# Performance work log

Hardware: AMD Instinct MI355X
Metric: run time of the kernel (lower is better)

## Reference

```python
import jax, jax.numpy as jnp
import numpy as np

B, L, J, CL, CJ, DM, NH, NB, OBS = 8192, 32, 31, 4, 8, 64, 4, 3, 128
TOK = CL * 16  # 64, flattened per-link token size
HD = DM // NH


def _ln(x, g, b):
    m = x.mean(-1, keepdims=True)
    v = ((x - m) ** 2).mean(-1, keepdims=True)
    return (x - m) / jnp.sqrt(v + 1e-5) * g + b


def setup_inputs() -> dict:
    key = jax.random.key(0)
    ks = list(jax.random.split(key, 30))
    rn = lambda k, s, sc=0.05: jax.random.normal(k, s, dtype=jnp.float32) * sc
    inp = {
        'obs': jax.random.normal(ks[0], (B, OBS), dtype=jnp.float32),
        # per-link MLP encoders (obs->64->TOK), stacked over links
        'link_enc_w1': rn(ks[1], (L, 64, OBS)),
        'link_enc_b1': jnp.zeros((L, 64), jnp.float32),
        'link_enc_w2': rn(ks[2], (L, TOK, 64)),
        'link_enc_b2': jnp.zeros((L, TOK), jnp.float32),
        # per-joint encoders (obs->CJ)
        'joint_enc_w': rn(ks[3], (J, CJ, OBS)),
        'joint_enc_b': jnp.zeros((J, CJ), jnp.float32),
        # Rodrigues kernels per block per joint
        'rod_mix': rn(ks[4], (NB, J, CL, CL), 0.2),
        'rod_theta_w': rn(ks[5], (NB, J, CL, CJ), 0.2),
        'rod_theta_b': jnp.zeros((NB, J, CL), jnp.float32),
        'rod_gen': rn(ks[6], (NB, J, 4, 4), 0.2),
        'rod_ln_g': jnp.ones((NB, L, TOK), jnp.float32),
        'rod_ln_b': jnp.zeros((NB, L, TOK), jnp.float32),
        # JointLayer linears per block per joint (TOK->CJ)
        'jl_w': rn(ks[7], (NB, J, CJ, TOK)),
        'jl_b': jnp.zeros((NB, J, CJ), jnp.float32),
        # attention per block
        'proj_in_w': rn(ks[8], (NB, DM, TOK)),
        'proj_in_b': jnp.zeros((NB, DM), jnp.float32),
        'qkv_w': rn(ks[9], (NB, 3 * DM, DM)),
        'qkv_b': jnp.zeros((NB, 3 * DM), jnp.float32),
        'attn_out_w': rn(ks[10], (NB, DM, DM)),
        'attn_out_b': jnp.zeros((NB, DM), jnp.float32),
        'proj_out_w': rn(ks[11], (NB, TOK, DM)),
        'proj_out_b': jnp.zeros((NB, TOK), jnp.float32),
        'attn_ln_g': jnp.ones((NB, TOK), jnp.float32),
        'attn_ln_b': jnp.zeros((NB, TOK), jnp.float32),
        # kinematic chain edges: parent j -> child j+1
        'p_idx': jnp.arange(J, dtype=jnp.int32),
        'c_idx': jnp.arange(1, J + 1, dtype=jnp.int32),
    }
    return inp


def _forward(obs, link_enc_w1, link_enc_b1, link_enc_w2, link_enc_b2,
             joint_enc_w, joint_enc_b, rod_mix, rod_theta_w, rod_theta_b,
             rod_gen, rod_ln_g, rod_ln_b, jl_w, jl_b, proj_in_w, proj_in_b,
             qkv_w, qkv_b, attn_out_w, attn_out_b, proj_out_w, proj_out_b,
             attn_ln_g, attn_ln_b, p_idx, c_idx):
    b = obs.shape[0]
    # ---- encode ----
    h = jax.nn.elu(jnp.einsum('bo,lho->blh', obs, link_enc_w1) + link_enc_b1)
    link = jnp.einsum('blh,lgh->blg', h, link_enc_w2) + link_enc_b2  # (B,L,TOK)
    link = link.reshape(b, L, CL, 4, 4)
    joint = jnp.einsum('bo,jco->bjc', obs, joint_enc_w) + joint_enc_b  # (B,J,CJ)
    for t in range(NB):
        # ---- RodriguesLayer (reads input link feats; unique children -> parallel) ----
        Fp = link[:, p_idx]  # (B,J,CL,4,4)
        Fc = link[:, c_idx]
        Fm = jnp.einsum('joc,bjcxy->bjoxy', rod_mix[t], Fp)
        a = jnp.einsum('bjc,joc->bjo', joint, rod_theta_w[t]) + rod_theta_b[t]  # (B,J,CL)
        G = rod_gen[t]
        GF = jnp.einsum('jxy,bjoyz->bjoxz', G, Fm)
        GGF = jnp.einsum('jxy,bjoyz->bjoxz', G, GF)
        s = jnp.sin(a)[..., None, None]
        c1 = (1.0 - jnp.cos(a))[..., None, None]
        Ft = Fm + s * GF + c1 * GGF  # Rodrigues: F + sin(a) G F + (1-cos(a)) G^2 F
        comb = _ln((Fc + Ft).reshape(b, J, TOK), rod_ln_g[t][c_idx], rod_ln_b[t][c_idx])
        root = _ln(link[:, 0].reshape(b, TOK), rod_ln_g[t][0], rod_ln_b[t][0])
        link = link.at[:, 0].set(root.reshape(b, CL, 4, 4))
        link = link.at[:, c_idx].set(comb.reshape(b, J, CL, 4, 4))
        # ---- JointLayer ----
        child_flat = link[:, c_idx].reshape(b, J, TOK)
        joint = jnp.einsum('bjh,jch->bjc', child_flat, jl_w[t]) + jl_b[t] + joint
        # ---- SelfAttentionLayer ----
        tok = link.reshape(b, L, TOK)
        x = jnp.einsum('blh,dh->bld', tok, proj_in_w[t]) + proj_in_b[t]
        qkv = jnp.einsum('bld,ed->ble', x, qkv_w[t]) + qkv_b[t]
        q, k, v = jnp.split(qkv, 3, axis=-1)
        hsplit = lambda z: z.reshape(b, L, NH, HD).transpose(0, 2, 1, 3)
        q, k, v = hsplit(q), hsplit(k), hsplit(v)
        attn = jax.nn.softmax(jnp.einsum('bhqd,bhkd->bhqk', q, k) / jnp.sqrt(jnp.float32(HD)), axis=-1)
        o = jnp.einsum('bhqk,bhkd->bhqd', attn, v).transpose(0, 2, 1, 3).reshape(b, L, DM)
        o = jnp.einsum('bld,ed->ble', o, attn_out_w[t]) + attn_out_b[t]
        o = jnp.einsum('bld,hd->blh', o, proj_out_w[t]) + proj_out_b[t]
        tok = _ln(tok + o, attn_ln_g[t], attn_ln_b[t])
        link = tok.reshape(b, L, CL, 4, 4)
    return jnp.concatenate([link.reshape(b, -1), joint.reshape(b, -1)], axis=-1)


def reference(obs, link_enc_w1, link_enc_b1, link_enc_w2, link_enc_b2,
              joint_enc_w, joint_enc_b, rod_mix, rod_theta_w, rod_theta_b,
              rod_gen, rod_ln_g, rod_ln_b, jl_w, jl_b, proj_in_w, proj_in_b,
              qkv_w, qkv_b, attn_out_w, attn_out_b, proj_out_w, proj_out_b,
              attn_ln_g, attn_ln_b, p_idx, c_idx):
    return _forward(obs, link_enc_w1, link_enc_b1, link_enc_w2, link_enc_b2,
                    joint_enc_w, joint_enc_b, rod_mix, rod_theta_w, rod_theta_b,
                    rod_gen, rod_ln_g, rod_ln_b, jl_w, jl_b, proj_in_w, proj_in_b,
                    qkv_w, qkv_b, attn_out_w, attn_out_b, proj_out_w, proj_out_b,
                    attn_ln_g, attn_ln_b, p_idx, c_idx)
```

## Files before the change

kernel.cpp:

```cpp
#include <hip/hip_runtime.h>

typedef unsigned short u16;
typedef __attribute__((ext_vector_type(8))) short bh8;
typedef __attribute__((ext_vector_type(4))) float fx4;

__device__ __forceinline__ u16 f2b(float f){
  unsigned int u = __float_as_uint(f);
  u += 0x7fffu + ((u>>16)&1u);
  return (u16)(u>>16);
}
__device__ __forceinline__ float b2f(u16 h){
  return __uint_as_float(((unsigned int)h)<<16);
}
__device__ __forceinline__ bh8 ldf(const u16* p){
  return *(const bh8*)p;
}
#define MFMA(a,b,c) __builtin_amdgcn_mfma_f32_16x16x32_bf16((a),(b),(c),0,0,0)

static const long OFF_W1 = 0;
static const long OFF_W2 = 278528;
static const long OFF_WJ = 425984;
static const long OFF_PI = 460800;
static const long OFF_QK = 474624;
static const long OFF_AO = 516096;
static const long OFF_PO = 529920;
static const long WS_U16 = 543744;

__global__ __launch_bounds__(256) void conv_kernel(
  const float* __restrict__ w1, const float* __restrict__ w2,
  const float* __restrict__ wj, const float* __restrict__ pi,
  const float* __restrict__ qk, const float* __restrict__ ao,
  const float* __restrict__ po, u16* __restrict__ ws)
{
  const int stride = gridDim.x*blockDim.x;
  const int g0 = blockIdx.x*blockDim.x + threadIdx.x;
  for (int i=g0;i<2048*136;i+=stride){ int r=i/136,c=i-r*136; ws[OFF_W1+i]= (c<128)? f2b(w1[(long)r*128+c]) : (u16)0; }
  for (int i=g0;i<2048*72;i+=stride){ int r=i/72,c=i-r*72; ws[OFF_W2+i]= (c<64)? f2b(w2[(long)(r<<6)+c]) : (u16)0; }
  for (int i=g0;i<256*136;i+=stride){ int r=i/136,c=i-r*136; ws[OFF_WJ+i]= (c<128&&r<248)? f2b(wj[(long)(r<<7)+c]) : (u16)0; }
  for (int i=g0;i<192*72;i+=stride){ int r=i/72,c=i-r*72; ws[OFF_PI+i]= (c<64)? f2b(pi[(r<<6)+c]) : (u16)0; }
  for (int i=g0;i<576*72;i+=stride){ int r=i/72,c=i-r*72; ws[OFF_QK+i]= (c<64)? f2b(qk[(r<<6)+c]) : (u16)0; }
  for (int i=g0;i<192*72;i+=stride){ int r=i/72,c=i-r*72; ws[OFF_AO+i]= (c<64)? f2b(ao[(r<<6)+c]) : (u16)0; }
  for (int i=g0;i<192*72;i+=stride){ int r=i/72,c=i-r*72; ws[OFF_PO+i]= (c<64)? f2b(po[(r<<6)+c]) : (u16)0; }
}

struct __align__(16) SMem1 {
  u16 obs_l[16][136];
  u16 wa[64][136];
  u16 wb[64][72];
  u16 hb[16][72];
};

template<bool PRE>
__global__ __launch_bounds__(256) void enc_kernel(
  const float* __restrict__ obs, const float* __restrict__ w1,
  const float* __restrict__ b1, const float* __restrict__ w2,
  const float* __restrict__ b2, const float* __restrict__ wj,
  const float* __restrict__ bj, const u16* __restrict__ wsw,
  float* __restrict__ dout)
{
  __shared__ SMem1 s;
  const int tid = threadIdx.x;
  const int wave = tid>>6, lane = tid&63;
  const int g = lane>>4, cc = lane&15;
  const long bb = (long)blockIdx.x*16;

  for (int i=tid;i<16*128;i+=256){ int r=i>>7,c=i&127; s.obs_l[r][c]=f2b(obs[(bb+r)*128+c]); }

  for (int l=0;l<32;l++){
    if (PRE){
      const u16* s1 = wsw + OFF_W1 + (long)l*8704;
      for (int i=tid*8;i<8704;i+=2048) *(bh8*)(&s.wa[0][0]+i) = *(const bh8*)(s1+i);
      const u16* s2 = wsw + OFF_W2 + (long)l*4608;
      for (int i=tid*8;i<4608;i+=2048) *(bh8*)(&s.wb[0][0]+i) = *(const bh8*)(s2+i);
    } else {
      for (int i=tid;i<64*128;i+=256){ s.wa[i>>7][i&127]=f2b(w1[(long)l*8192+i]); }
      for (int i=tid;i<64*64;i+=256){ s.wb[i>>6][i&63]=f2b(w2[(long)l*4096+i]); }
    }
    __syncthreads();
    {
      fx4 acc = {0.f,0.f,0.f,0.f};
      #pragma unroll
      for (int ks=0;ks<4;ks++)
        acc = MFMA(ldf(&s.obs_l[cc][ks*32+g*8]), ldf(&s.wa[wave*16+cc][ks*32+g*8]), acc);
      int col = wave*16+cc;
      float bias = b1[l*64+col];
      #pragma unroll
      for (int r=0;r<4;r++){
        float v = acc[r]+bias;
        v = v>0.f ? v : expm1f(v);
        s.hb[g*4+r][col] = f2b(v);
      }
    }
    __syncthreads();
    {
      fx4 acc = {0.f,0.f,0.f,0.f};
      #pragma unroll
      for (int ks=0;ks<2;ks++)
        acc = MFMA(ldf(&s.hb[cc][ks*32+g*8]), ldf(&s.wb[wave*16+cc][ks*32+g*8]), acc);
      int col = wave*16+cc;
      float bias = b2[l*64+col];
      #pragma unroll
      for (int r=0;r<4;r++)
        dout[(bb+g*4+r)*2296 + l*64 + col] = acc[r]+bias;
    }
    __syncthreads();
  }
  for (int ci=0;ci<4;ci++){
    if (PRE){
      const u16* sj = wsw + OFF_WJ + (long)ci*8704;
      for (int i=tid*8;i<8704;i+=2048) *(bh8*)(&s.wa[0][0]+i) = *(const bh8*)(sj+i);
    } else {
      for (int i=tid;i<64*128;i+=256){
        int r=i>>7,c=i&127; int grow=ci*64+r;
        s.wa[r][c] = (grow<248)? f2b(wj[(long)grow*128+c]) : (u16)0;
      }
    }
    __syncthreads();
    fx4 acc={0.f,0.f,0.f,0.f};
    #pragma unroll
    for (int ks=0;ks<4;ks++)
      acc = MFMA(ldf(&s.obs_l[cc][ks*32+g*8]), ldf(&s.wa[wave*16+cc][ks*32+g*8]), acc);
    int ncol = ci*64 + wave*16 + cc;
    if (ncol<248){
      float bias = bj[ncol];
      #pragma unroll
      for (int r=0;r<4;r++)
        dout[(bb+g*4+r)*2296 + 2048 + ncol] = acc[r]+bias;
    }
    __syncthreads();
  }
}

struct __align__(16) SMem2 {
  float tokf[4][32][68];
  u16   tokb[4][32][72];
  u16   xs[4*32*72];
  u16   qs[4*32*72];
  u16   kk[4*32*72];
  u16   vT[4][64][40];
  float joint[4][31][8];
  union {
    u16 w[192*72];
    u16 p[8][32][40];
  } u;
};
static_assert(sizeof(SMem2) <= 163840, "LDS overflow");

template<int NT, class EPI>
__device__ __forceinline__ void gemm8(const u16* A, const u16* W,
                                      int wave, int lane, EPI epi){
  const int g = lane>>4, cc = lane&15;
  const int row = wave*16 + cc;
  bh8 a0 = ldf(&A[row*72 + g*8]);
  bh8 a1 = ldf(&A[row*72 + 32 + g*8]);
  #pragma unroll
  for (int nt=0;nt<NT;nt++){
    bh8 b0 = ldf(&W[(nt*16+cc)*72 + g*8]);
    bh8 b1 = ldf(&W[(nt*16+cc)*72 + 32 + g*8]);
    fx4 acc = {0.f,0.f,0.f,0.f};
    acc = MFMA(a0,b0,acc);
    acc = MFMA(a1,b1,acc);
    epi(nt, wave, acc);
  }
}

template<bool PRE>
__device__ __forceinline__ void stageW(u16* dst, const u16* wsrc, const float* fsrc, int rows){
  if (PRE){
    const int n = rows*72;
    for (int i=threadIdx.x*8; i<n; i+=4096)
      *(bh8*)(dst+i) = *(const bh8*)(wsrc+i);
  } else {
    const int n = rows*64;
    for (int i=threadIdx.x; i<n; i+=512)
      dst[(i>>6)*72 + (i&63)] = f2b(fsrc[i]);
  }
}

template<bool PRE>
__global__ __launch_bounds__(512,1) void rodri_main(
  const float* __restrict__ rod_mix, const float* __restrict__ rod_theta_w,
  const float* __restrict__ rod_theta_b, const float* __restrict__ rod_gen,
  const float* __restrict__ rod_ln_g, const float* __restrict__ rod_ln_b,
  const float* __restrict__ jl_w, const float* __restrict__ jl_b,
  const float* __restrict__ proj_in_w, const float* __restrict__ proj_in_b,
  const float* __restrict__ qkv_w, const float* __restrict__ qkv_b,
  const float* __restrict__ attn_out_w, const float* __restrict__ attn_out_b,
  const float* __restrict__ proj_out_w, const float* __restrict__ proj_out_b,
  const float* __restrict__ attn_ln_g, const float* __restrict__ attn_ln_b,
  const u16* __restrict__ wsw, float* __restrict__ dout)
{
  __shared__ SMem2 s;
  const int tid = threadIdx.x;
  const int wave = tid>>6, lane = tid&63;
  const int g = lane>>4, cc = lane&15;
  const long bb = (long)blockIdx.x*4;

  for (int i=tid;i<4*2048;i+=512){
    int b=i>>11, r=i&2047;
    float v = dout[(bb+b)*2296 + r];
    s.tokf[b][r>>6][r&63] = v;
    s.tokb[b][r>>6][r&63] = f2b(v);
  }
  for (int i=tid;i<4*248;i+=512){
    int b=i/248, r=i-b*248;
    s.joint[b][r>>3][r&7] = dout[(bb+b)*2296 + 2048 + r];
  }
  __syncthreads();

  for (int t=0;t<3;t++){
    {
      const int unit = tid>>2, o = tid&3;
      const int b = unit>>5, row = unit&31;
      float nv[16];
      if (row == 0){
        #pragma unroll
        for (int i=0;i<16;i++) nv[i] = s.tokf[b][0][o*16+i];
      } else {
        const int j = row-1;
        const long wj = (long)t*31 + j;
        const float* mixp = rod_mix + wj*16 + o*4;
        const float* thwp = rod_theta_w + wj*32 + o*8;
        const float* genp = rod_gen + wj*16;
        float a = rod_theta_b[wj*4+o];
        #pragma unroll
        for (int c8=0;c8<8;c8++) a += s.joint[b][j][c8]*thwp[c8];
        float sn = sinf(a), c1 = 1.f - cosf(a);
        const float m0 = mixp[0], m1 = mixp[1], m2 = mixp[2], m3 = mixp[3];
        float G[16];
        #pragma unroll
        for (int e=0;e<16;e++) G[e] = genp[e];
        #pragma unroll
        for (int z=0;z<4;z++){
          float fm[4], gf[4], gg[4];
          #pragma unroll
          for (int x=0;x<4;x++)
            fm[x] = m0*s.tokf[b][j][     x*4+z] + m1*s.tokf[b][j][16 + x*4+z]
                  + m2*s.tokf[b][j][32 + x*4+z] + m3*s.tokf[b][j][48 + x*4+z];
          #pragma unroll
          for (int x=0;x<4;x++)
            gf[x] = G[x*4+0]*fm[0] + G[x*4+1]*fm[1] + G[x*4+2]*fm[2] + G[x*4+3]*fm[3];
          #pragma unroll
          for (int x=0;x<4;x++)
            gg[x] = G[x*4+0]*gf[0] + G[x*4+1]*gf[1] + G[x*4+2]*gf[2] + G[x*4+3]*gf[3];
          #pragma unroll
          for (int x=0;x<4;x++)
            nv[x*4+z] = fm[x] + sn*gf[x] + c1*gg[x] + s.tokf[b][row][o*16+x*4+z];
        }
      }
      float sum=0.f, ssq=0.f;
      #pragma unroll
      for (int i=0;i<16;i++){ sum+=nv[i]; ssq+=nv[i]*nv[i]; }
      sum += __shfl_xor(sum,1); ssq += __shfl_xor(ssq,1);
      sum += __shfl_xor(sum,2); ssq += __shfl_xor(ssq,2);
      float mean = sum*(1.f/64.f);
      float var  = ssq*(1.f/64.f) - mean*mean;
      float rstd = rsqrtf(var + 1e-5f);
      const float* lng = rod_ln_g + ((long)t*32+row)*64 + o*16;
      const float* lnb = rod_ln_b + ((long)t*32+row)*64 + o*16;
      #pragma unroll
      for (int i=0;i<16;i++)
        nv[i] = (nv[i]-mean)*rstd*lng[i] + lnb[i];
      __syncthreads();
      #pragma unroll
      for (int i=0;i<16;i++){
        s.tokf[b][row][o*16+i] = nv[i];
        s.tokb[b][row][o*16+i] = f2b(nv[i]);
      }
    }
    __syncthreads();

    if (tid < 248){
      int j = tid>>3, c8 = tid&7;
      const float* wrow = jl_w + (((long)t*31 + j)*8 + c8)*64;
      float bias = jl_b[((long)t*31+j)*8 + c8];
      float a0=0.f,a1=0.f,a2=0.f,a3=0.f;
      for (int h=0;h<64;h++){
        float w = wrow[h];
        a0 += w*b2f(s.tokb[0][j+1][h]);
        a1 += w*b2f(s.tokb[1][j+1][h]);
        a2 += w*b2f(s.tokb[2][j+1][h]);
        a3 += w*b2f(s.tokb[3][j+1][h]);
      }
      s.joint[0][j][c8] += a0 + bias;
      s.joint[1][j][c8] += a1 + bias;
      s.joint[2][j][c8] += a2 + bias;
      s.joint[3][j][c8] += a3 + bias;
    }
    __syncthreads();

    stageW<PRE>(s.u.w, wsw+OFF_PI+(long)t*4608, proj_in_w+(long)t*4096, 64);
    __syncthreads();
    {
      const float* bp = proj_in_b + (long)t*64;
      gemm8<4>(&s.tokb[0][0][0], s.u.w, wave, lane,
        [&](int nt,int mtile,const fx4& acc){
          int col = nt*16+cc;
          float bias = bp[col];
          #pragma unroll
          for (int r=0;r<4;r++){
            int rg = mtile*16+g*4+r;
            s.xs[rg*72+col] = f2b(acc[r]+bias);
          }
        });
    }
    __syncthreads();

    stageW<PRE>(s.u.w, wsw+OFF_QK+(long)t*13824, qkv_w+(long)t*12288, 192);
    __syncthreads();
    {
      const float* bq = qkv_b + (long)t*192;
      gemm8<12>(s.xs, s.u.w, wave, lane,
        [&](int nt,int mtile,const fx4& acc){
          int col = nt*16+cc;
          float bias = bq[col];
          #pragma unroll
          for (int r=0;r<4;r++){
            int rg = mtile*16+g*4+r;
            float v = acc[r]+bias;
            int b = rg>>5, l = rg&31;
            if (col<64)       s.qs[rg*72+col]      = f2b(v);
            else if (col<128) s.kk[rg*72+(col-64)] = f2b(v);
            else              s.vT[b][col-128][l]  = f2b(v);
          }
        });
    }
    __syncthreads();

    {
      const int b = wave>>1;
      const u16* qb = s.qs + b*32*72;
      const u16* kb = s.kk + b*32*72;
      u16* ob = s.xs + b*32*72;
      bh8 z8 = {0,0,0,0,0,0,0,0};
      #pragma unroll
      for (int hh=0;hh<2;hh++){
        const int h = (wave&1) + 2*hh;
        bh8 qf[2], kf[2];
        #pragma unroll
        for (int it=0;it<2;it++)
          qf[it] = (g<2) ? ldf(&qb[(it*16+cc)*72 + h*16 + g*8]) : z8;
        #pragma unroll
        for (int jt=0;jt<2;jt++)
          kf[jt] = (g<2) ? ldf(&kb[(jt*16+cc)*72 + h*16 + g*8]) : z8;
        fx4 sacc[2][2];
        #pragma unroll
        for (int it=0;it<2;it++)
          #pragma unroll
          for (int jt=0;jt<2;jt++){
            fx4 z = {0.f,0.f,0.f,0.f};
            sacc[it][jt] = MFMA(qf[it], kf[jt], z);
          }
        float pn[2][2][4];
        #pragma unroll
        for (int it=0;it<2;it++)
          #pragma unroll
          for (int r=0;r<4;r++){
            float v0 = sacc[it][0][r], v1 = sacc[it][1][r];
            float m = fmaxf(v0,v1);
            #pragma unroll
            for (int msk=1; msk<16; msk<<=1) m = fmaxf(m, __shfl_xor(m,msk));
            float e0 = __expf((v0-m)*0.25f);
            float e1 = __expf((v1-m)*0.25f);
            float sm = e0+e1;
            #pragma unroll
            for (int msk=1; msk<16; msk<<=1) sm += __shfl_xor(sm,msk);
            float inv = 1.f/sm;
            pn[it][0][r]=e0*inv; pn[it][1][r]=e1*inv;
          }
        #pragma unroll
        for (int it=0;it<2;it++)
          #pragma unroll
          for (int jt=0;jt<2;jt++)
            #pragma unroll
            for (int r=0;r<4;r++)
              s.u.p[wave][it*16+g*4+r][jt*16+cc] = f2b(pn[it][jt][r]);
        bh8 vf = ldf(&s.vT[b][h*16+cc][g*8]);
        #pragma unroll
        for (int it=0;it<2;it++){
          bh8 pf = ldf(&s.u.p[wave][it*16+cc][g*8]);
          fx4 z = {0.f,0.f,0.f,0.f};
          fx4 oacc = MFMA(pf, vf, z);
          #pragma unroll
          for (int r=0;r<4;r++)
            ob[(it*16+g*4+r)*72 + h*16+cc] = f2b(oacc[r]);
        }
      }
    }
    __syncthreads();

    stageW<PRE>(s.u.w, wsw+OFF_AO+(long)t*4608, attn_out_w+(long)t*4096, 64);
    __syncthreads();
    {
      const float* bo = attn_out_b + (long)t*64;
      gemm8<4>(s.xs, s.u.w, wave, lane,
        [&](int nt,int mtile,const fx4& acc){
          int col = nt*16+cc;
          float bias = bo[col];
          #pragma unroll
          for (int r=0;r<4;r++){
            int rg = mtile*16+g*4+r;
            s.qs[rg*72+col] = f2b(acc[r]+bias);
          }
        });
    }
    __syncthreads();

    stageW<PRE>(s.u.w, wsw+OFF_PO+(long)t*4608, proj_out_w+(long)t*4096, 64);
    __syncthreads();
    {
      const float* bp2 = proj_out_b + (long)t*64;
      gemm8<4>(s.qs, s.u.w, wave, lane,
        [&](int nt,int mtile,const fx4& acc){
          int col = nt*16+cc;
          float bias = bp2[col];
          #pragma unroll
          for (int r=0;r<4;r++){
            int rg = mtile*16+g*4+r;
            int b = rg>>5, l = rg&31;
            s.tokf[b][l][col] += acc[r] + bias;
          }
        });
    }
    __syncthreads();

    {
      const int unit = tid>>2, o = tid&3;
      const int b = unit>>5, row = unit&31;
      float v[16];
      #pragma unroll
      for (int i=0;i<16;i++) v[i] = s.tokf[b][row][o*16+i];
      float sum=0.f, ssq=0.f;
      #pragma unroll
      for (int i=0;i<16;i++){ sum+=v[i]; ssq+=v[i]*v[i]; }
      sum += __shfl_xor(sum,1); ssq += __shfl_xor(ssq,1);
      sum += __shfl_xor(sum,2); ssq += __shfl_xor(ssq,2);
      float mean = sum*(1.f/64.f);
      float var  = ssq*(1.f/64.f) - mean*mean;
      float rstd = rsqrtf(var + 1e-5f);
      const float* lg = attn_ln_g + (long)t*64 + o*16;
      const float* lb = attn_ln_b + (long)t*64 + o*16;
      #pragma unroll
      for (int i=0;i<16;i++){
        float ov = (v[i]-mean)*rstd*lg[i] + lb[i];
        s.tokf[b][row][o*16+i] = ov;
        s.tokb[b][row][o*16+i] = f2b(ov);
      }
    }
    __syncthreads();
  }

  for (int i=tid;i<4*2048;i+=512){
    int b=i>>11, r=i&2047;
    dout[(bb+b)*2296 + r] = s.tokf[b][r>>6][r&63];
  }
  for (int i=tid;i<4*248;i+=512){
    int b=i/248, r=i-b*248;
    dout[(bb+b)*2296 + 2048 + r] = s.joint[b][r>>3][r&7];
  }
}

extern "C" void kernel_launch(void* const* d_in, const int* in_sizes, int n_in,
                              void* d_out, int out_size, void* d_ws, size_t ws_size,
                              hipStream_t stream) {
  (void)in_sizes; (void)n_in; (void)out_size;
  float* out = (float*)d_out;
  u16* ws = (u16*)d_ws;
  const bool pre = (ws_size >= (size_t)WS_U16*2);

  if (pre){
    conv_kernel<<<dim3(512), dim3(256), 0, stream>>>(
      (const float*)d_in[1], (const float*)d_in[3], (const float*)d_in[5],
      (const float*)d_in[15], (const float*)d_in[17], (const float*)d_in[19],
      (const float*)d_in[21], ws);
    enc_kernel<true><<<dim3(512), dim3(256), 0, stream>>>(
      (const float*)d_in[0], (const float*)d_in[1], (const float*)d_in[2],
      (const float*)d_in[3], (const float*)d_in[4], (const float*)d_in[5],
      (const float*)d_in[6], ws, out);
    rodri_main<true><<<dim3(2048), dim3(512), 0, stream>>>(
      (const float*)d_in[7],  (const float*)d_in[8],  (const float*)d_in[9],
      (const float*)d_in[10], (const float*)d_in[11], (const float*)d_in[12],
      (const float*)d_in[13], (const float*)d_in[14], (const float*)d_in[15],
      (const float*)d_in[16], (const float*)d_in[17], (const float*)d_in[18],
      (const float*)d_in[19], (const float*)d_in[20], (const float*)d_in[21],
      (const float*)d_in[22], (const float*)d_in[23], (const float*)d_in[24],
      ws, out);
  } else {
    enc_kernel<false><<<dim3(512), dim3(256), 0, stream>>>(
      (const float*)d_in[0], (const float*)d_in[1], (const float*)d_in[2],
      (const float*)d_in[3], (const float*)d_in[4], (const float*)d_in[5],
      (const float*)d_in[6], ws, out);
    rodri_main<false><<<dim3(2048), dim3(512), 0, stream>>>(
      (const float*)d_in[7],  (const float*)d_in[8],  (const float*)d_in[9],
      (const float*)d_in[10], (const float*)d_in[11], (const float*)d_in[12],
      (const float*)d_in[13], (const float*)d_in[14], (const float*)d_in[15],
      (const float*)d_in[16], (const float*)d_in[17], (const float*)d_in[18],
      (const float*)d_in[19], (const float*)d_in[20], (const float*)d_in[21],
      (const float*)d_in[22], (const float*)d_in[23], (const float*)d_in[24],
      ws, out);
  }
}
```

Measured before the change: 528.9 us.

## Fold proj_in into QKV and attn_out into proj_out weights

The prep kernel now precomputes the products qkv_w·proj_in_w and proj_out_w·attn_out_w, along with their combined biases, and stores them in the workspace. The main kernel then runs one 192-wide GEMM directly on the tokens for Q/K/V and one 64-wide GEMM for the output projection. This removes two GEMMs, their weight staging and several block-wide barriers per block iteration. In exchange the folded weights are rounded to bf16 once as a product, which changes the rounding relative to the reference's two-step computation. The non-workspace fallback keeps the original unfolded path.

After: 485.6 us. 1.09x faster.

```diff
diff --git a/kernel.cpp b/kernel.cpp
--- a/kernel.cpp
+++ b/kernel.cpp
@@ -24,13 +24,20 @@
 static const long OFF_QK = 474624;
 static const long OFF_AO = 516096;
 static const long OFF_PO = 529920;
-static const long WS_U16 = 543744;
+static const long OFF_QP = 543744;
+static const long OFF_OP = 585216;
+static const long OFF_BQ = 599040;
+static const long OFF_BO = 600192;
+static const long WS_U16 = 600576;
 
 __global__ __launch_bounds__(256) void conv_kernel(
   const float* __restrict__ w1, const float* __restrict__ w2,
-  const float* __restrict__ wj, const float* __restrict__ pi,
-  const float* __restrict__ qk, const float* __restrict__ ao,
-  const float* __restrict__ po, u16* __restrict__ ws)
+  const float* __restrict__ wj,
+  const float* __restrict__ pi, const float* __restrict__ pib,
+  const float* __restrict__ qk, const float* __restrict__ qkb,
+  const float* __restrict__ ao, const float* __restrict__ aob,
+  const float* __restrict__ po, const float* __restrict__ pob,
+  u16* __restrict__ ws)
 {
   const int stride = gridDim.x*blockDim.x;
   const int g0 = blockIdx.x*blockDim.x + threadIdx.x;
@@ -41,6 +48,43 @@
   for (int i=g0;i<576*72;i+=stride){ int r=i/72,c=i-r*72; ws[OFF_QK+i]= (c<64)? f2b(qk[(r<<6)+c]) : (u16)0; }
   for (int i=g0;i<192*72;i+=stride){ int r=i/72,c=i-r*72; ws[OFF_AO+i]= (c<64)? f2b(ao[(r<<6)+c]) : (u16)0; }
   for (int i=g0;i<192*72;i+=stride){ int r=i/72,c=i-r*72; ws[OFF_PO+i]= (c<64)? f2b(po[(r<<6)+c]) : (u16)0; }
+
+  for (int i=g0;i<3*192*64;i+=stride){
+    int t=i/(192*64), rem=i-t*192*64, e=rem>>6, h=rem&63;
+    const float* qw = qk + ((long)t*192+e)*64;
+    const float* pw = pi + (long)t*4096 + h;
+    float acc=0.f;
+    #pragma unroll 8
+    for (int d=0;d<64;d++) acc += qw[d]*pw[d*64];
+    ws[OFF_QP + (long)t*13824 + e*72 + h] = f2b(acc);
+  }
+  for (int i=g0;i<3*192;i+=stride){
+    int t=i/192, e=i-t*192;
+    const float* qw = qk + ((long)t*192+e)*64;
+    const float* pb = pib + (long)t*64;
+    float acc = qkb[(long)t*192+e];
+    #pragma unroll 8
+    for (int d=0;d<64;d++) acc += qw[d]*pb[d];
+    ((float*)(ws+OFF_BQ))[i] = acc;
+  }
+  for (int i=g0;i<3*64*64;i+=stride){
+    int t=i/(64*64), rem=i-t*64*64, n=rem>>6, d=rem&63;
+    const float* pw = po + (long)t*4096 + (long)n*64;
+    const float* aw = ao + (long)t*4096 + d;
+    float acc=0.f;
+    #pragma unroll 8
+    for (int e=0;e<64;e++) acc += pw[e]*aw[e*64];
+    ws[OFF_OP + (long)t*4608 + n*72 + d] = f2b(acc);
+  }
+  for (int i=g0;i<3*64;i+=stride){
+    int t=i/64, n=i-t*64;
+    const float* pw = po + (long)t*4096 + (long)n*64;
+    const float* ab = aob + (long)t*64;
+    float acc = pob[(long)t*64+n];
+    #pragma unroll 8
+    for (int e=0;e<64;e++) acc += pw[e]*ab[e];
+    ((float*)(ws+OFF_BO))[i] = acc;
+  }
 }
 
 struct __align__(16) SMem1 {
@@ -177,16 +221,162 @@
   }
 }
 
-template<bool PRE>
-__global__ __launch_bounds__(512,1) void rodri_main(
+__device__ __forceinline__ void rodrigues_phase(SMem2& s, int t, int tid,
+  const float* __restrict__ rod_mix, const float* __restrict__ rod_theta_w,
+  const float* __restrict__ rod_theta_b, const float* __restrict__ rod_gen,
+  const float* __restrict__ rod_ln_g, const float* __restrict__ rod_ln_b)
+{
+  const int unit = tid>>2, o = tid&3;
+  const int b = unit>>5, row = unit&31;
+  float nv[16];
+  if (row == 0){
+    #pragma unroll
+    for (int i=0;i<16;i++) nv[i] = s.tokf[b][0][o*16+i];
+  } else {
+    const int j = row-1;
+    const long wj = (long)t*31 + j;
+    const float* mixp = rod_mix + wj*16 + o*4;
+    const float* thwp = rod_theta_w + wj*32 + o*8;
+    const float* genp = rod_gen + wj*16;
+    float a = rod_theta_b[wj*4+o];
+    #pragma unroll
+    for (int c8=0;c8<8;c8++) a += s.joint[b][j][c8]*thwp[c8];
+    float sn = sinf(a), c1 = 1.f - cosf(a);
+    const float m0 = mixp[0], m1 = mixp[1], m2 = mixp[2], m3 = mixp[3];
+    float G[16];
+    #pragma unroll
+    for (int e=0;e<16;e++) G[e] = genp[e];
+    #pragma unroll
+    for (int z=0;z<4;z++){
+      float fm[4], gf[4], gg[4];
+      #pragma unroll
+      for (int x=0;x<4;x++)
+        fm[x] = m0*s.tokf[b][j][     x*4+z] + m1*s.tokf[b][j][16 + x*4+z]
+              + m2*s.tokf[b][j][32 + x*4+z] + m3*s.tokf[b][j][48 + x*4+z];
+      #pragma unroll
+      for (int x=0;x<4;x++)
+        gf[x] = G[x*4+0]*fm[0] + G[x*4+1]*fm[1] + G[x*4+2]*fm[2] + G[x*4+3]*fm[3];
+      #pragma unroll
+      for (int x=0;x<4;x++)
+        gg[x] = G[x*4+0]*gf[0] + G[x*4+1]*gf[1] + G[x*4+2]*gf[2] + G[x*4+3]*gf[3];
+      #pragma unroll
+      for (int x=0;x<4;x++)
+        nv[x*4+z] = fm[x] + sn*gf[x] + c1*gg[x] + s.tokf[b][row][o*16+x*4+z];
+    }
+  }
+  float sum=0.f, ssq=0.f;
+  #pragma unroll
+  for (int i=0;i<16;i++){ sum+=nv[i]; ssq+=nv[i]*nv[i]; }
+  sum += __shfl_xor(sum,1); ssq += __shfl_xor(ssq,1);
+  sum += __shfl_xor(sum,2); ssq += __shfl_xor(ssq,2);
+  float mean = sum*(1.f/64.f);
+  float var  = ssq*(1.f/64.f) - mean*mean;
+  float rstd = rsqrtf(var + 1e-5f);
+  const float* lng = rod_ln_g + ((long)t*32+row)*64 + o*16;
+  const float* lnb = rod_ln_b + ((long)t*32+row)*64 + o*16;
+  #pragma unroll
+  for (int i=0;i<16;i++)
+    nv[i] = (nv[i]-mean)*rstd*lng[i] + lnb[i];
+  __syncthreads();
+  #pragma unroll
+  for (int i=0;i<16;i++){
+    s.tokf[b][row][o*16+i] = nv[i];
+    s.tokb[b][row][o*16+i] = f2b(nv[i]);
+  }
+}
+
+__device__ __forceinline__ void attn_phase(SMem2& s, int wave, int g, int cc){
+  const int b = wave>>1;
+  const u16* qb = s.qs + b*32*72;
+  const u16* kb = s.kk + b*32*72;
+  u16* ob = s.xs + b*32*72;
+  bh8 z8 = {0,0,0,0,0,0,0,0};
+  #pragma unroll
+  for (int hh=0;hh<2;hh++){
+    const int h = (wave&1) + 2*hh;
+    bh8 qf[2], kf[2];
+    #pragma unroll
+    for (int it=0;it<2;it++)
+      qf[it] = (g<2) ? ldf(&qb[(it*16+cc)*72 + h*16 + g*8]) : z8;
+    #pragma unroll
+    for (int jt=0;jt<2;jt++)
+      kf[jt] = (g<2) ? ldf(&kb[(jt*16+cc)*72 + h*16 + g*8]) : z8;
+    fx4 sacc[2][2];
+    #pragma unroll
+    for (int it=0;it<2;it++)
+      #pragma unroll
+      for (int jt=0;jt<2;jt++){
+        fx4 z = {0.f,0.f,0.f,0.f};
+        sacc[it][jt] = MFMA(qf[it], kf[jt], z);
+      }
+    float pn[2][2][4];
+    #pragma unroll
+    for (int it=0;it<2;it++)
+      #pragma unroll
+      for (int r=0;r<4;r++){
+        float v0 = sacc[it][0][r], v1 = sacc[it][1][r];
+        float m = fmaxf(v0,v1);
+        #pragma unroll
+        for (int msk=1; msk<16; msk<<=1) m = fmaxf(m, __shfl_xor(m,msk));
+        float e0 = __expf((v0-m)*0.25f);
+        float e1 = __expf((v1-m)*0.25f);
+        float sm = e0+e1;
+        #pragma unroll
+        for (int msk=1; msk<16; msk<<=1) sm += __shfl_xor(sm,msk);
+        float inv = 1.f/sm;
+        pn[it][0][r]=e0*inv; pn[it][1][r]=e1*inv;
+      }
+    #pragma unroll
+    for (int it=0;it<2;it++)
+      #pragma unroll
+      for (int jt=0;jt<2;jt++)
+        #pragma unroll
+        for (int r=0;r<4;r++)
+          s.u.p[wave][it*16+g*4+r][jt*16+cc] = f2b(pn[it][jt][r]);
+    bh8 vf = ldf(&s.vT[b][h*16+cc][g*8]);
+    #pragma unroll
+    for (int it=0;it<2;it++){
+      bh8 pf = ldf(&s.u.p[wave][it*16+cc][g*8]);
+      fx4 z = {0.f,0.f,0.f,0.f};
+      fx4 oacc = MFMA(pf, vf, z);
+      #pragma unroll
+      for (int r=0;r<4;r++)
+        ob[(it*16+g*4+r)*72 + h*16+cc] = f2b(oacc[r]);
+    }
+  }
+}
+
+__device__ __forceinline__ void attnln_phase(SMem2& s, int t, int tid,
+  const float* __restrict__ attn_ln_g, const float* __restrict__ attn_ln_b)
+{
+  const int unit = tid>>2, o = tid&3;
+  const int b = unit>>5, row = unit&31;
+  float v[16];
+  #pragma unroll
+  for (int i=0;i<16;i++) v[i] = s.tokf[b][row][o*16+i];
+  float sum=0.f, ssq=0.f;
+  #pragma unroll
+  for (int i=0;i<16;i++){ sum+=v[i]; ssq+=v[i]*v[i]; }
+  sum += __shfl_xor(sum,1); ssq += __shfl_xor(ssq,1);
+  sum += __shfl_xor(sum,2); ssq += __shfl_xor(ssq,2);
+  float mean = sum*(1.f/64.f);
+  float var  = ssq*(1.f/64.f) - mean*mean;
+  float rstd = rsqrtf(var + 1e-5f);
+  const float* lg = attn_ln_g + (long)t*64 + o*16;
+  const float* lb = attn_ln_b + (long)t*64 + o*16;
+  #pragma unroll
+  for (int i=0;i<16;i++){
+    float ov = (v[i]-mean)*rstd*lg[i] + lb[i];
+    s.tokf[b][row][o*16+i] = ov;
+    s.tokb[b][row][o*16+i] = f2b(ov);
+  }
+}
+
+__global__ __launch_bounds__(512,1) void rodri_fold(
   const float* __restrict__ rod_mix, const float* __restrict__ rod_theta_w,
   const float* __restrict__ rod_theta_b, const float* __restrict__ rod_gen,
   const float* __restrict__ rod_ln_g, const float* __restrict__ rod_ln_b,
   const float* __restrict__ jl_w, const float* __restrict__ jl_b,
-  const float* __restrict__ proj_in_w, const float* __restrict__ proj_in_b,
-  const float* __restrict__ qkv_w, const float* __restrict__ qkv_b,
-  const float* __restrict__ attn_out_w, const float* __restrict__ attn_out_b,
-  const float* __restrict__ proj_out_w, const float* __restrict__ proj_out_b,
   const float* __restrict__ attn_ln_g, const float* __restrict__ attn_ln_b,
   const u16* __restrict__ wsw, float* __restrict__ dout)
 {
@@ -209,65 +399,7 @@
   __syncthreads();
 
   for (int t=0;t<3;t++){
-    {
-      const int unit = tid>>2, o = tid&3;
-      const int b = unit>>5, row = unit&31;
-      float nv[16];
-      if (row == 0){
-        #pragma unroll
-        for (int i=0;i<16;i++) nv[i] = s.tokf[b][0][o*16+i];
-      } else {
-        const int j = row-1;
-        const long wj = (long)t*31 + j;
-        const float* mixp = rod_mix + wj*16 + o*4;
-        const float* thwp = rod_theta_w + wj*32 + o*8;
-        const float* genp = rod_gen + wj*16;
-        float a = rod_theta_b[wj*4+o];
-        #pragma unroll
-        for (int c8=0;c8<8;c8++) a += s.joint[b][j][c8]*thwp[c8];
-        float sn = sinf(a), c1 = 1.f - cosf(a);
-        const float m0 = mixp[0], m1 = mixp[1], m2 = mixp[2], m3 = mixp[3];
-        float G[16];
-        #pragma unroll
-        for (int e=0;e<16;e++) G[e] = genp[e];
-        #pragma unroll
-        for (int z=0;z<4;z++){
-          float fm[4], gf[4], gg[4];
-          #pragma unroll
-          for (int x=0;x<4;x++)
-            fm[x] = m0*s.tokf[b][j][     x*4+z] + m1*s.tokf[b][j][16 + x*4+z]
-                  + m2*s.tokf[b][j][32 + x*4+z] + m3*s.tokf[b][j][48 + x*4+z];
-          #pragma unroll
-          for (int x=0;x<4;x++)
-            gf[x] = G[x*4+0]*fm[0] + G[x*4+1]*fm[1] + G[x*4+2]*fm[2] + G[x*4+3]*fm[3];
-          #pragma unroll
-          for (int x=0;x<4;x++)
-            gg[x] = G[x*4+0]*gf[0] + G[x*4+1]*gf[1] + G[x*4+2]*gf[2] + G[x*4+3]*gf[3];
-          #pragma unroll
-          for (int x=0;x<4;x++)
-            nv[x*4+z] = fm[x] + sn*gf[x] + c1*gg[x] + s.tokf[b][row][o*16+x*4+z];
-        }
-      }
-      float sum=0.f, ssq=0.f;
-      #pragma unroll
-      for (int i=0;i<16;i++){ sum+=nv[i]; ssq+=nv[i]*nv[i]; }
-      sum += __shfl_xor(sum,1); ssq += __shfl_xor(ssq,1);
-      sum += __shfl_xor(sum,2); ssq += __shfl_xor(ssq,2);
-      float mean = sum*(1.f/64.f);
-      float var  = ssq*(1.f/64.f) - mean*mean;
-      float rstd = rsqrtf(var + 1e-5f);
-      const float* lng = rod_ln_g + ((long)t*32+row)*64 + o*16;
-      const float* lnb = rod_ln_b + ((long)t*32+row)*64 + o*16;
-      #pragma unroll
-      for (int i=0;i<16;i++)
-        nv[i] = (nv[i]-mean)*rstd*lng[i] + lnb[i];
-      __syncthreads();
-      #pragma unroll
-      for (int i=0;i<16;i++){
-        s.tokf[b][row][o*16+i] = nv[i];
-        s.tokb[b][row][o*16+i] = f2b(nv[i]);
-      }
-    }
+    rodrigues_phase(s, t, tid, rod_mix, rod_theta_w, rod_theta_b, rod_gen, rod_ln_g, rod_ln_b);
     __syncthreads();
 
     if (tid < 248){
@@ -289,7 +421,116 @@
     }
     __syncthreads();
 
-    stageW<PRE>(s.u.w, wsw+OFF_PI+(long)t*4608, proj_in_w+(long)t*4096, 64);
+    stageW<true>(s.u.w, wsw+OFF_QP+(long)t*13824, nullptr, 192);
+    __syncthreads();
+    {
+      const float* bq = (const float*)(wsw + OFF_BQ) + (long)t*192;
+      gemm8<12>(&s.tokb[0][0][0], s.u.w, wave, lane,
+        [&](int nt,int mtile,const fx4& acc){
+          int col = nt*16+cc;
+          float bias = bq[col];
+          #pragma unroll
+          for (int r=0;r<4;r++){
+            int rg = mtile*16+g*4+r;
+            float v = acc[r]+bias;
+            int b = rg>>5, l = rg&31;
+            if (col<64)       s.qs[rg*72+col]      = f2b(v);
+            else if (col<128) s.kk[rg*72+(col-64)] = f2b(v);
+            else              s.vT[b][col-128][l]  = f2b(v);
+          }
+        });
+    }
+    __syncthreads();
+
+    attn_phase(s, wave, g, cc);
+    __syncthreads();
+
+    stageW<true>(s.u.w, wsw+OFF_OP+(long)t*4608, nullptr, 64);
+    __syncthreads();
+    {
+      const float* bo = (const float*)(wsw + OFF_BO) + (long)t*64;
+      gemm8<4>(s.xs, s.u.w, wave, lane,
+        [&](int nt,int mtile,const fx4& acc){
+          int col = nt*16+cc;
+          float bias = bo[col];
+          #pragma unroll
+          for (int r=0;r<4;r++){
+            int rg = mtile*16+g*4+r;
+            int b = rg>>5, l = rg&31;
+            s.tokf[b][l][col] += acc[r] + bias;
+          }
+        });
+    }
+    __syncthreads();
+
+    attnln_phase(s, t, tid, attn_ln_g, attn_ln_b);
+    __syncthreads();
+  }
+
+  for (int i=tid;i<4*2048;i+=512){
+    int b=i>>11, r=i&2047;
+    dout[(bb+b)*2296 + r] = s.tokf[b][r>>6][r&63];
+  }
+  for (int i=tid;i<4*248;i+=512){
+    int b=i/248, r=i-b*248;
+    dout[(bb+b)*2296 + 2048 + r] = s.joint[b][r>>3][r&7];
+  }
+}
+
+__global__ __launch_bounds__(512,1) void rodri_nopre(
+  const float* __restrict__ rod_mix, const float* __restrict__ rod_theta_w,
+  const float* __restrict__ rod_theta_b, const float* __restrict__ rod_gen,
+  const float* __restrict__ rod_ln_g, const float* __restrict__ rod_ln_b,
+  const float* __restrict__ jl_w, const float* __restrict__ jl_b,
+  const float* __restrict__ proj_in_w, const float* __restrict__ proj_in_b,
+  const float* __restrict__ qkv_w, const float* __restrict__ qkv_b,
+  const float* __restrict__ attn_out_w, const float* __restrict__ attn_out_b,
+  const float* __restrict__ proj_out_w, const float* __restrict__ proj_out_b,
+  const float* __restrict__ attn_ln_g, const float* __restrict__ attn_ln_b,
+  float* __restrict__ dout)
+{
+  __shared__ SMem2 s;
+  const int tid = threadIdx.x;
+  const int wave = tid>>6, lane = tid&63;
+  const int g = lane>>4, cc = lane&15;
+  const long bb = (long)blockIdx.x*4;
+
+  for (int i=tid;i<4*2048;i+=512){
+    int b=i>>11, r=i&2047;
+    float v = dout[(bb+b)*2296 + r];
+    s.tokf[b][r>>6][r&63] = v;
+    s.tokb[b][r>>6][r&63] = f2b(v);
+  }
+  for (int i=tid;i<4*248;i+=512){
+    int b=i/248, r=i-b*248;
+    s.joint[b][r>>3][r&7] = dout[(bb+b)*2296 + 2048 + r];
+  }
+  __syncthreads();
+
+  for (int t=0;t<3;t++){
+    rodrigues_phase(s, t, tid, rod_mix, rod_theta_w, rod_theta_b, rod_gen, rod_ln_g, rod_ln_b);
+    __syncthreads();
+
+    if (tid < 248){
+      int j = tid>>3, c8 = tid&7;
+      const float* wrow = jl_w + (((long)t*31 + j)*8 + c8)*64;
+      float bias = jl_b[((long)t*31+j)*8 + c8];
+      float a0=0.f,a1=0.f,a2=0.f,a3=0.f;
+      for (int h=0;h<64;h++){
+        float w = wrow[h];
+        a0 += w*b2f(s.tokb[0][j+1][h]);
+        a1 += w*b2f(s.tokb[1][j+1][h]);
+        a2 += w*b2f(s.tokb[2][j+1][h]);
+        a3 += w*b2f(s.tokb[3][j+1][h]);
+      }
+      s.joint[0][j][c8] += a0 + bias;
+      s.joint[1][j][c8] += a1 + bias;
+      s.joint[2][j][c8] += a2 + bias;
+      s.joint[3][j][c8] += a3 + bias;
+    }
+    __syncthreads();
+
+    stageW<false>(s.u.w, nullptr, proj_in_w+(long)t*4096, 64);
     __syncthreads();
     {
       const float* bp = proj_in_b + (long)t*64;
@@ -306,7 +547,7 @@
     }
     __syncthreads();
 
-    stageW<PRE>(s.u.w, wsw+OFF_QK+(long)t*13824, qkv_w+(long)t*12288, 192);
+    stageW<false>(s.u.w, nullptr, qkv_w+(long)t*12288, 192);
     __syncthreads();
     {
       const float* bq = qkv_b + (long)t*192;
@@ -327,69 +568,10 @@
     }
     __syncthreads();
 
-    {
-      const int b = wave>>1;
-      const u16* qb = s.qs + b*32*72;
-      const u16* kb = s.kk + b*32*72;
-      u16* ob = s.xs + b*32*72;
-      bh8 z8 = {0,0,0,0,0,0,0,0};
-      #pragma unroll
-      for (int hh=0;hh<2;hh++){
-        const int h = (wave&1) + 2*hh;
-        bh8 qf[2], kf[2];
-        #pragma unroll
-        for (int it=0;it<2;it++)
-          qf[it] = (g<2) ? ldf(&qb[(it*16+cc)*72 + h*16 + g*8]) : z8;
-        #pragma unroll
-        for (int jt=0;jt<2;jt++)
-          kf[jt] = (g<2) ? ldf(&kb[(jt*16+cc)*72 + h*16 + g*8]) : z8;
-        fx4 sacc[2][2];
-        #pragma unroll
-        for (int it=0;it<2;it++)
-          #pragma unroll
-          for (int jt=0;jt<2;jt++){
-            fx4 z = {0.f,0.f,0.f,0.f};
-            sacc[it][jt] = MFMA(qf[it], kf[jt], z);
-          }
-        float pn[2][2][4];
-        #pragma unroll
-        for (int it=0;it<2;it++)
-          #pragma unroll
-          for (int r=0;r<4;r++){
-            float v0 = sacc[it][0][r], v1 = sacc[it][1][r];
-            float m = fmaxf(v0,v1);
-            #pragma unroll
-            for (int msk=1; msk<16; msk<<=1) m = fmaxf(m, __shfl_xor(m,msk));
-            float e0 = __expf((v0-m)*0.25f);
-            float e1 = __expf((v1-m)*0.25f);
-            float sm = e0+e1;
-            #pragma unroll
-            for (int msk=1; msk<16; msk<<=1) sm += __shfl_xor(sm,msk);
-            float inv = 1.f/sm;
-            pn[it][0][r]=e0*inv; pn[it][1][r]=e1*inv;
-          }
-        #pragma unroll
-        for (int it=0;it<2;it++)
-          #pragma unroll
-          for (int jt=0;jt<2;jt++)
-            #pragma unroll
-            for (int r=0;r<4;r++)
-              s.u.p[wave][it*16+g*4+r][jt*16+cc] = f2b(pn[it][jt][r]);
-        bh8 vf = ldf(&s.vT[b][h*16+cc][g*8]);
-        #pragma unroll
-        for (int it=0;it<2;it++){
-          bh8 pf = ldf(&s.u.p[wave][it*16+cc][g*8]);
-          fx4 z = {0.f,0.f,0.f,0.f};
-          fx4 oacc = MFMA(pf, vf, z);
-          #pragma unroll
-          for (int r=0;r<4;r++)
-            ob[(it*16+g*4+r)*72 + h*16+cc] = f2b(oacc[r]);
-        }
-      }
-    }
-    __syncthreads();
-
-    stageW<PRE>(s.u.w, wsw+OFF_AO+(long)t*4608, attn_out_w+(long)t*4096, 64);
+    attn_phase(s, wave, g, cc);
+    __syncthreads();
+
+    stageW<false>(s.u.w, nullptr, attn_out_w+(long)t*4096, 64);
     __syncthreads();
     {
       const float* bo = attn_out_b + (long)t*64;
@@ -406,7 +588,7 @@
     }
     __syncthreads();
 
-    stageW<PRE>(s.u.w, wsw+OFF_PO+(long)t*4608, proj_out_w+(long)t*4096, 64);
+    stageW<false>(s.u.w, nullptr, proj_out_w+(long)t*4096, 64);
     __syncthreads();
     {
       const float* bp2 = proj_out_b + (long)t*64;
@@ -424,29 +606,7 @@
     }
     __syncthreads();
 
-    {
-      const int unit = tid>>2, o = tid&3;
-      const int b = unit>>5, row = unit&31;
-      float v[16];
-      #pragma unroll
-      for (int i=0;i<16;i++) v[i] = s.tokf[b][row][o*16+i];
-      float sum=0.f, ssq=0.f;
-      #pragma unroll
-      for (int i=0;i<16;i++){ sum+=v[i]; ssq+=v[i]*v[i]; }
-      sum += __shfl_xor(sum,1); ssq += __shfl_xor(ssq,1);
-      sum += __shfl_xor(sum,2); ssq += __shfl_xor(ssq,2);
-      float mean = sum*(1.f/64.f);
-      float var  = ssq*(1.f/64.f) - mean*mean;
-      float rstd = rsqrtf(var + 1e-5f);
-      const float* lg = attn_ln_g + (long)t*64 + o*16;
-      const float* lb = attn_ln_b + (long)t*64 + o*16;
-      #pragma unroll
-      for (int i=0;i<16;i++){
-        float ov = (v[i]-mean)*rstd*lg[i] + lb[i];
-        s.tokf[b][row][o*16+i] = ov;
-        s.tokb[b][row][o*16+i] = f2b(ov);
-      }
-    }
+    attnln_phase(s, t, tid, attn_ln_g, attn_ln_b);
     __syncthreads();
   }
 
@@ -471,32 +631,32 @@
   if (pre){
     conv_kernel<<<dim3(512), dim3(256), 0, stream>>>(
       (const float*)d_in[1], (const float*)d_in[3], (const float*)d_in[5],
-      (const float*)d_in[15], (const float*)d_in[17], (const float*)d_in[19],
-      (const float*)d_in[21], ws);
+      (const float*)d_in[15], (const float*)d_in[16],
+      (const float*)d_in[17], (const float*)d_in[18],
+      (const float*)d_in[19], (const float*)d_in[20],
+      (const float*)d_in[21], (const float*)d_in[22], ws);
     enc_kernel<true><<<dim3(512), dim3(256), 0, stream>>>(
       (const float*)d_in[0], (const float*)d_in[1], (const float*)d_in[2],
       (const float*)d_in[3], (const float*)d_in[4], (const float*)d_in[5],
       (const float*)d_in[6], ws, out);
-    rodri_main<true><<<dim3(2048), dim3(512), 0, stream>>>(
+    rodri_fold<<<dim3(2048), dim3(512), 0, stream>>>(
+      (const float*)d_in[7],  (const float*)d_in[8],  (const float*)d_in[9],
+      (const float*)d_in[10], (const float*)d_in[11], (const float*)d_in[12],
+      (const float*)d_in[13], (const float*)d_in[14],
+      (const float*)d_in[23], (const float*)d_in[24],
+      ws, out);
+  } else {
+    enc_kernel<false><<<dim3(512), dim3(256), 0, stream>>>(
+      (const float*)d_in[0], (const float*)d_in[1], (const float*)d_in[2],
+      (const float*)d_in[3], (const float*)d_in[4], (const float*)d_in[5],
+      (const float*)d_in[6], ws, out);
+    rodri_nopre<<<dim3(2048), dim3(512), 0, stream>>>(
       (const float*)d_in[7],  (const float*)d_in[8],  (const float*)d_in[9],
       (const float*)d_in[10], (const float*)d_in[11], (const float*)d_in[12],
       (const float*)d_in[13], (const float*)d_in[14], (const float*)d_in[15],
       (const float*)d_in[16], (const float*)d_in[17], (const float*)d_in[18],
       (const float*)d_in[19], (const float*)d_in[20], (const float*)d_in[21],
       (const float*)d_in[22], (const float*)d_in[23], (const float*)d_in[24],
-      ws, out);
-  } else {
-    enc_kernel<false><<<dim3(512), dim3(256), 0, stream>>>(
-      (const float*)d_in[0], (const float*)d_in[1], (const float*)d_in[2],
-      (const float*)d_in[3], (const float*)d_in[4], (const float*)d_in[5],
-      (const float*)d_in[6], ws, out);
-    rodri_main<false><<<dim3(2048), dim3(512), 0, stream>>>(
-      (const float*)d_in[7],  (const float*)d_in[8],  (const float*)d_in[9],
-      (const float*)d_in[10], (const float*)d_in[11], (const float*)d_in[12],
-      (const float*)d_in[13], (const float*)d_in[14], (const float*)d_in[15],
-      (const float*)d_in[16], (const float*)d_in[17], (const float*)d_in[18],
-      (const float*)d_in[19], (const float*)d_in[20], (const float*)d_in[21],
-      (const float*)d_in[22], (const float*)d_in[23], (const float*)d_in[24],
-      ws, out);
-  }
-}
+      out);
+  }
+}
```
